# Performance work log

Hardware: AMD Instinct MI355X
Metric: run time of the kernel (lower is better)

## Reference

```python
import jax, jax.numpy as jnp
import numpy as np

B, T, IN = 128, 2048, 32      # batch, seq_len, input dim
S, M = 32, 8                  # kaarma state dim, number of ensemble models
E, H = 64, 128                # encoder dim, controller GRU hidden
CIN = E + 1                   # controller input = [encoded, error]


def setup_inputs() -> dict:
    key = jax.random.key(0)
    ks = jax.random.split(key, 15)
    sc = 0.1  # small init scale keeps tanh/sigmoid in sane range
    return {
        "x": jax.random.normal(ks[0], (B, T, IN), jnp.float32),
        "y": jax.random.normal(ks[1], (B, T), jnp.float32),
        # mkaarma params: shared encoder + per-model recurrent state update
        "W_enc": jax.random.normal(ks[2], (IN, E), jnp.float32) * sc,
        "b_enc": jnp.zeros((E,), jnp.float32),
        "W_in": jax.random.normal(ks[3], (M, IN, S), jnp.float32) * sc,
        "W_rec": jax.random.normal(ks[4], (M, S, S), jnp.float32) * sc,
        "b_s": jnp.zeros((M, S), jnp.float32),
        # controller params: GRU cell + gate head
        "W_x": jax.random.normal(ks[5], (CIN, 3 * H), jnp.float32) * sc,
        "W_h": jax.random.normal(ks[6], (H, 3 * H), jnp.float32) * sc,
        "b_x": jnp.zeros((3 * H,), jnp.float32),
        "b_h": jnp.zeros((3 * H,), jnp.float32),
        "W_gate": jax.random.normal(ks[7], (H, M), jnp.float32) * sc,
        "b_gate": jnp.zeros((M,), jnp.float32),
    }


def reference(x, y, W_enc, b_enc, W_in, W_rec, b_s,
              W_x, W_h, b_x, b_h, W_gate, b_gate):
    Bv = x.shape[0]
    dt = x.dtype

    def step(carry, xy):
        kstate, h, err = carry            # [B,S], [B,H], [B]
        x_t, y_t = xy                     # [B,IN], [B]
        # mkaarma: encode input + ensemble of candidate next states
        encoded = jnp.tanh(x_t @ W_enc + b_enc)                        # [B,E]
        new_state = jnp.tanh(
            jnp.einsum('bi,mis->bms', x_t, W_in)
            + jnp.einsum('bs,msd->bmd', kstate, W_rec)
            + b_s
        )                                                              # [B,M,S]
        # controller: GRU cell on [encoded, error]
        inp = jnp.concatenate([encoded, err[:, None]], axis=1)         # [B,E+1]
        xz, xr, xn = jnp.split(inp @ W_x + b_x, 3, axis=1)
        hz, hr, hn = jnp.split(h @ W_h + b_h, 3, axis=1)
        z = jax.nn.sigmoid(xz + hz)
        r = jax.nn.sigmoid(xr + hr)
        n = jnp.tanh(xn + r * hn)
        h_new = (1.0 - z) * n + z * h                                  # [B,H]
        # gate softmax over models, mix candidate states
        gate = jax.nn.softmax(h_new @ W_gate + b_gate, axis=1)         # [B,M]
        kstate_new = jnp.einsum('bm,bms->bs', gate, new_state)         # [B,S]
        pred = kstate_new[:, -1]                                       # [B]
        err_new = pred - y_t
        return (kstate_new, h_new, err_new), pred

    init = (jnp.zeros((Bv, S), dt), jnp.zeros((Bv, H), dt), jnp.zeros((Bv,), dt))
    xs = (jnp.swapaxes(x, 0, 1), jnp.swapaxes(y, 0, 1))   # time-major
    _, preds = jax.lax.scan(step, init, xs)               # [T,B]
    return jnp.swapaxes(preds, 0, 1)                      # [B,T]
```

## Files before the change

kernel.cpp:

```cpp
#include <hip/hip_runtime.h>

typedef _Float16 h2 __attribute__((ext_vector_type(2)));
typedef _Float16 h8 __attribute__((ext_vector_type(8)));

#define NB 128
#define NT 2048
#define NIN 32
#define NS 32
#define NM 8
#define NE 64
#define NH 128
#define NH3 384

__device__ __forceinline__ h2 mkh2(float a, float b) {
  h2 r; r[0] = (_Float16)a; r[1] = (_Float16)b; return r;
}

template <int I>
__device__ __forceinline__ h2 pick2(h8 v) {
  return __builtin_shufflevector(v, v, 2 * I, 2 * I + 1);
}

__device__ __forceinline__ float fdot2(h2 a, h2 b, float c) {
#if __has_builtin(__builtin_amdgcn_fdot2)
  return __builtin_amdgcn_fdot2(a, b, c, false);
#else
  return c + (float)a[0] * (float)b[0] + (float)a[1] * (float)b[1];
#endif
}

__device__ __forceinline__ float rcpf(float v) {
#if __has_builtin(__builtin_amdgcn_rcpf)
  return __builtin_amdgcn_rcpf(v);
#else
  return 1.0f / v;
#endif
}

__device__ __forceinline__ float sigmoid_f(float v) { return rcpf(1.0f + __expf(-v)); }
__device__ __forceinline__ float tanh_f(float v) { return 1.0f - 2.0f * rcpf(1.0f + __expf(2.0f * v)); }

template <int CTRL>
__device__ __forceinline__ float dppadd(float v) {
  int t = __builtin_amdgcn_update_dpp(0, __float_as_int(v), CTRL, 0xF, 0xF, true);
  return v + __int_as_float(t);
}
__device__ __forceinline__ float wave_reduce63(float v) {
  v = dppadd<0x111>(v); v = dppadd<0x112>(v); v = dppadd<0x114>(v);
  v = dppadd<0x118>(v); v = dppadd<0x142>(v); v = dppadd<0x143>(v);
  return v;
}
__device__ __forceinline__ float pairsum(float v) {
  int t = __builtin_amdgcn_update_dpp(0, __float_as_int(v), 0xB1, 0xF, 0xF, true);
  return v + __int_as_float(t);
}

__device__ __forceinline__ void lds_fence() {
  asm volatile("s_waitcnt lgkmcnt(0)" ::: "memory");
}

__device__ __forceinline__ void softbar() {
  asm volatile("s_waitcnt lgkmcnt(0)\n\ts_barrier" ::: "memory");
}

#define RPW 16
__global__ __launch_bounds__(256, 1) void pre2(
    const float* __restrict__ gx, const float* __restrict__ W_enc,
    const float* __restrict__ b_enc, const float* __restrict__ W_x,
    const float* __restrict__ b_x, _Float16* __restrict__ xpre,
    _Float16* __restrict__ xh16, int t0, int CH) {
  const int tid = threadIdx.x, wv = tid >> 6, lane = tid & 63;
  __shared__ __align__(16) _Float16 x16[4][NIN];
  __shared__ __align__(16) _Float16 encA[4][RPW][NE];

  h2 we[16];
#pragma unroll
  for (int i = 0; i < 16; ++i)
    we[i] = mkh2(W_enc[(2 * i) * NE + lane], W_enc[(2 * i + 1) * NE + lane]);
  const float be = b_enc[lane];

  const int g0 = ((int)blockIdx.x * 4 + wv) * RPW;

  h2 wx3[96];
#pragma unroll 1
  for (int pass = 0; pass < 2; ++pass) {
#pragma unroll
    for (int kk = 0; kk < 3; ++kk) {
      const int j = lane + 64 * (3 * pass + kk);
#pragma unroll
      for (int i = 0; i < 32; ++i)
        wx3[kk * 32 + i] = mkh2(W_x[(size_t)(2 * i) * NH3 + j], W_x[(size_t)(2 * i + 1) * NH3 + j]);
    }
#pragma unroll 1
    for (int r = 0; r < RPW; ++r) {
      const int g = g0 + r;
      const int bb = g / CH, tc = g % CH;
      if (pass == 0) {
        const float* xr = gx + ((size_t)bb * NT + t0 + tc) * NIN;
        if (lane < NIN) x16[wv][lane] = (_Float16)xr[lane];
        lds_fence();
        if (lane < 16) {
          const unsigned v = *(const unsigned*)&x16[wv][2 * lane];
          ((unsigned*)xh16)[(size_t)g * 16 + lane] = v;
        }
        const h8* xv8 = (const h8*)x16[wv];
        float a = be;
#pragma unroll
        for (int i = 0; i < 4; ++i) {
          const h8 xv = xv8[i];
          a = fdot2(pick2<0>(xv), we[4 * i + 0], a);
          a = fdot2(pick2<1>(xv), we[4 * i + 1], a);
          a = fdot2(pick2<2>(xv), we[4 * i + 2], a);
          a = fdot2(pick2<3>(xv), we[4 * i + 3], a);
        }
        encA[wv][r][lane] = (_Float16)tanh_f(a);
        lds_fence();
      }
      const h8* ev8 = (const h8*)encA[wv][r];
      h8 ev[8];
#pragma unroll
      for (int i = 0; i < 8; ++i) ev[i] = ev8[i];
#pragma unroll
      for (int kk = 0; kk < 3; ++kk) {
        const int j = lane + 64 * (3 * pass + kk);
        float a = b_x[j], c = 0.f;
#pragma unroll
        for (int i = 0; i < 8; ++i) {
          a = fdot2(pick2<0>(ev[i]), wx3[kk * 32 + 4 * i + 0], a);
          c = fdot2(pick2<1>(ev[i]), wx3[kk * 32 + 4 * i + 1], c);
          a = fdot2(pick2<2>(ev[i]), wx3[kk * 32 + 4 * i + 2], a);
          c = fdot2(pick2<3>(ev[i]), wx3[kk * 32 + 4 * i + 3], c);
        }
        xpre[(size_t)g * NH3 + j] = (_Float16)(a + c);
      }
    }
  }
}

__global__ __launch_bounds__(384, 2) void rnn8(
    const float* __restrict__ gy, const _Float16* __restrict__ xpre,
    const _Float16* __restrict__ xh16,
    const float* __restrict__ W_h, const float* __restrict__ b_h,
    const float* __restrict__ W_in, const float* __restrict__ W_rec,
    const float* __restrict__ b_s, const float* __restrict__ W_x,
    const float* __restrict__ W_gate, const float* __restrict__ b_gate,
    float* __restrict__ out, float* __restrict__ state, int t0, int CH) {
  const int tid = threadIdx.x;
  const int b = blockIdx.x;
  const int wv = tid >> 6;
  const int lane = tid & 63;

  __shared__ __align__(16) _Float16 h_sh[2][NH];
  __shared__ __align__(16) _Float16 xpre_sh[2][NH3];
  __shared__ __align__(16) float ns_sh[2][NS][NM];
  __shared__ __align__(16) float xd_sh[2][2 * NH];
  __shared__ __align__(16) float gp_sh[2][4][NM];
  __shared__ __align__(16) _Float16 kst_sh[NS];
  __shared__ float err_sh;
  __shared__ float y_lds[NT];

  float* st = state + b * (NH + NS + 1);

  h2 wbig[96];
  h2 wrec[16];
  float wg[8];
  float bh[3], wxe[3];
  float bs4[4];
  float bg[8];
  float h_prev = 0.f;
  unsigned xpq[12];
  h8 xr0[4], xr1[4], xr2[4], xr3[4];

  const int gl = tid - 128;
  const int j = gl >> 1;
  const int half = gl & 1;

  for (int i = tid; i < CH; i += 384) y_lds[i] = gy[(size_t)b * NT + t0 + i];

  if (wv >= 2) {
#pragma unroll
    for (int g = 0; g < 3; ++g) {
      const int jc = j + 128 * g;
#pragma unroll
      for (int i = 0; i < 32; ++i)
        wbig[g * 32 + i] = mkh2(W_h[(size_t)(64 * half + 2 * i) * NH3 + jc],
                                W_h[(size_t)(64 * half + 2 * i + 1) * NH3 + jc]);
      bh[g] = b_h[jc];
      wxe[g] = W_x[(size_t)NE * NH3 + jc];
    }
#pragma unroll
    for (int m = 0; m < 8; ++m) wg[m] = half ? 0.f : W_gate[j * NM + m];
    {
      const int m0 = gl >> 5, d0 = gl & 31;
#pragma unroll
      for (int i = 0; i < 16; ++i)
        wrec[i] = mkh2(W_rec[m0 * 1024 + (2 * i) * 32 + d0],
                       W_rec[m0 * 1024 + (2 * i + 1) * 32 + d0]);
    }
    h_prev = t0 ? st[j] : 0.f;
    if (!half) h_sh[1][j] = (_Float16)h_prev;
  } else if (wv == 1) {
#pragma unroll
    for (int k = 0; k < 4; ++k) {
      const int o = lane + 64 * k, m = o >> 5, d = o & 31;
#pragma unroll
      for (int i = 0; i < 16; ++i)
        wbig[k * 16 + i] = mkh2(W_in[m * 1024 + (2 * i) * 32 + d],
                                W_in[m * 1024 + (2 * i + 1) * 32 + d]);
      bs4[k] = b_s[o];
    }
    {
      const h8* x0 = (const h8*)(xh16 + (size_t)(b * CH) * NIN);
#pragma unroll
      for (int i = 0; i < 4; ++i) xr0[i] = x0[i];
#pragma unroll
      for (int k = 0; k < 4; ++k) {
        float s = bs4[k];
#pragma unroll
        for (int i = 0; i < 4; ++i) {
          s = fdot2(pick2<0>(xr0[i]), wbig[k * 16 + 4 * i + 0], s);
          s = fdot2(pick2<1>(xr0[i]), wbig[k * 16 + 4 * i + 1], s);
          s = fdot2(pick2<2>(xr0[i]), wbig[k * 16 + 4 * i + 2], s);
          s = fdot2(pick2<3>(xr0[i]), wbig[k * 16 + 4 * i + 3], s);
        }
        xd_sh[1][lane + 64 * k] = s;
      }
    }
  } else {
#pragma unroll
    for (int m = 0; m < 8; ++m) bg[m] = b_gate[m];
    if (lane < NS) kst_sh[lane] = t0 ? (_Float16)st[NH + lane] : (_Float16)0.f;
    if (lane == 0) err_sh = t0 ? st[NH + NS] : 0.f;
  }
  __syncthreads();

  float hz = 0.f, hr = 0.f, hn = 0.f;

#define STEPK(K, XRK)                                                          \
  {                                                                            \
    const int tc = tc4 + (K);                                                  \
    const int q = (K) & 1, qp = q ^ 1;                                         \
                                 \
    if (wv >= 2) {                                                             \
      const h8* hv8 = (const h8*)&h_sh[qp][64 * half];                         \
      float a0 = 0.f, c0 = 0.f, a1 = 0.f, c1 = 0.f, a2 = 0.f, c2 = 0.f;        \
      _Pragma("unroll")                                                        \
      for (int i = 0; i < 8; ++i) {                                            \
        const h8 hv = hv8[i];                                                  \
        a0 = fdot2(pick2<0>(hv), wbig[4 * i + 0], a0);                         \
        c0 = fdot2(pick2<1>(hv), wbig[4 * i + 1], c0);                         \
        a0 = fdot2(pick2<2>(hv), wbig[4 * i + 2], a0);                         \
        c0 = fdot2(pick2<3>(hv), wbig[4 * i + 3], c0);                         \
        a1 = fdot2(pick2<0>(hv), wbig[32 + 4 * i + 0], a1);                    \
        c1 = fdot2(pick2<1>(hv), wbig[32 + 4 * i + 1], c1);                    \
        a1 = fdot2(pick2<2>(hv), wbig[32 + 4 * i + 2], a1);                    \
        c1 = fdot2(pick2<3>(hv), wbig[32 + 4 * i + 3], c1);                    \
        a2 = fdot2(pick2<0>(hv), wbig[64 + 4 * i + 0], a2);                    \
        c2 = fdot2(pick2<1>(hv), wbig[64 + 4 * i + 1], c2);                    \
        a2 = fdot2(pick2<2>(hv), wbig[64 + 4 * i + 2], a2);                    \
        c2 = fdot2(pick2<3>(hv), wbig[64 + 4 * i + 3], c2);                    \
      }                                                                        \
      hz = pairsum(a0 + c0) + bh[0];                                           \
      hr = pairsum(a1 + c1) + bh[1];                                           \
      hn = pairsum(a2 + c2) + bh[2];                                           \
    } else if (wv == 0) {                                                      \
      if (tc > 0) {                                                            \
        const int u = lane & 31;                                               \
        const float4* nsv = (const float4*)&ns_sh[qp][u][0];                   \
        const float4 n0 = nsv[0], n1 = nsv[1];                                 \
        const float4* g4 = (const float4*)&gp_sh[qp][0][0];                    \
        float4 A = g4[0], Bv = g4[1];                                          \
        A.x += g4[2].x + g4[4].x + g4[6].x; A.y += g4[2].y + g4[4].y + g4[6].y;\
        A.z += g4[2].z + g4[4].z + g4[6].z; A.w += g4[2].w + g4[4].w + g4[6].w;\
        Bv.x += g4[3].x + g4[5].x + g4[7].x; Bv.y += g4[3].y + g4[5].y + g4[7].y;\
        Bv.z += g4[3].z + g4[5].z + g4[7].z; Bv.w += g4[3].w + g4[5].w + g4[7].w;\
        float l[8] = {A.x + bg[0], A.y + bg[1], A.z + bg[2], A.w + bg[3],      \
                      Bv.x + bg[4], Bv.y + bg[5], Bv.z + bg[6], Bv.w + bg[7]}; \
        float mx = fmaxf(fmaxf(fmaxf(l[0], l[1]), fmaxf(l[2], l[3])),          \
                         fmaxf(fmaxf(l[4], l[5]), fmaxf(l[6], l[7])));         \
        float e[8], s = 0.f;                                                   \
        _Pragma("unroll")                                                      \
        for (int m = 0; m < 8; ++m) { e[m] = __expf(l[m] - mx); s += e[m]; }   \
        float ks = e[0] * n0.x + e[1] * n0.y + e[2] * n0.z + e[3] * n0.w +     \
                   e[4] * n1.x + e[5] * n1.y + e[6] * n1.z + e[7] * n1.w;      \
        ks *= rcpf(s);                                                         \
        if (lane < NS) kst_sh[u] = (_Float16)ks;                               \
        if (lane == 31) {                                                      \
          out[(size_t)b * NT + t0 + tc - 1] = ks;                              \
          err_sh = ks - y_lds[tc - 1];                                         \
        }                                                                      \
      }                                                                        \
    } else {    \
      if ((K) == 0) {                                                          \
        const unsigned* xpg = (const unsigned*)xpre;                           \
        _Pragma("unroll")                                                      \
        for (int k = 0; k < 4; ++k) {                                          \
          const size_t rr = (size_t)(b * CH + tc4 + k) * 192;                  \
          xpq[3 * k + 0] = xpg[rr + lane];                                     \
          xpq[3 * k + 1] = xpg[rr + lane + 64];                                \
          xpq[3 * k + 2] = xpg[rr + lane + 128];                               \
        }                                                                      \
        const h8* xg0 = (const h8*)(xh16 + (size_t)(b * CH + min(tc4 + 1, CH - 1)) * NIN); \
        const h8* xg1 = (const h8*)(xh16 + (size_t)(b * CH + min(tc4 + 2, CH - 1)) * NIN); \
        const h8* xg2 = (const h8*)(xh16 + (size_t)(b * CH + min(tc4 + 3, CH - 1)) * NIN); \
        const h8* xg3 = (const h8*)(xh16 + (size_t)(b * CH + min(tc4 + 4, CH - 1)) * NIN); \
        _Pragma("unroll")                                                      \
        for (int i = 0; i < 4; ++i) {                                          \
          xr0[i] = xg0[i]; xr1[i] = xg1[i]; xr2[i] = xg2[i]; xr3[i] = xg3[i];  \
        }                                                                      \
      }                                                                        \
      unsigned* xps = (unsigned*)&xpre_sh[q][0];                               \
      xps[lane] = xpq[3 * (K) + 0];                                            \
      xps[lane + 64] = xpq[3 * (K) + 1];                                       \
      xps[lane + 128] = xpq[3 * (K) + 2];                                      \
    }                                                                          \
    softbar();                                                                 \
                                 \
    if (wv >= 2) {                                                             \
      const float err = err_sh;                                                \
      const float xz = (float)xpre_sh[q][j] + err * wxe[0];                    \
      const float xr = (float)xpre_sh[q][j + 128] + err * wxe[1];              \
      const float xn = (float)xpre_sh[q][j + 256] + err * wxe[2];              \
      const float z = sigmoid_f(hz + xz);                                      \
      const float r = sigmoid_f(hr + xr);                                      \
      const float n = tanh_f(xn + r * hn);                                     \
      const float hnew = (1.f - z) * n + z * h_prev;                           \
      h_prev = hnew;                                                           \
      if (!half) h_sh[q][j] = (_Float16)hnew;                                  \
      float p[8];                                                              \
      _Pragma("unroll")                                                        \
      for (int m = 0; m < 8; ++m) p[m] = wave_reduce63(hnew * wg[m]);          \
      if (lane == 63) {                                                        \
        *(float4*)&gp_sh[q][wv - 2][0] = make_float4(p[0], p[1], p[2], p[3]);  \
        *(float4*)&gp_sh[q][wv - 2][4] = make_float4(p[4], p[5], p[6], p[7]);  \
      }                                                                        \
      const h8* kv8 = (const h8*)kst_sh;                                       \
      float s = xd_sh[qp][gl];                                                 \
      _Pragma("unroll")                                                        \
      for (int i = 0; i < 4; ++i) {                                            \
        const h8 kv = kv8[i];                                                  \
        s = fdot2(pick2<0>(kv), wrec[4 * i + 0], s);                           \
        s = fdot2(pick2<1>(kv), wrec[4 * i + 1], s);                           \
        s = fdot2(pick2<2>(kv), wrec[4 * i + 2], s);                           \
        s = fdot2(pick2<3>(kv), wrec[4 * i + 3], s);                           \
      }                                                                        \
      ns_sh[q][gl & 31][gl >> 5] = tanh_f(s);                                  \
    } else if (wv == 1) {                                                      \
      if (tc + 1 < CH) {                                                       \
        _Pragma("unroll")                                                      \
        for (int k = 0; k < 4; ++k) {                                          \
          float s = bs4[k];                                                    \
          _Pragma("unroll")                                                    \
          for (int i = 0; i < 4; ++i) {                                        \
            s = fdot2(pick2<0>(XRK[i]), wbig[k * 16 + 4 * i + 0], s);          \
            s = fdot2(pick2<1>(XRK[i]), wbig[k * 16 + 4 * i + 1], s);          \
            s = fdot2(pick2<2>(XRK[i]), wbig[k * 16 + 4 * i + 2], s);          \
            s = fdot2(pick2<3>(XRK[i]), wbig[k * 16 + 4 * i + 3], s);          \
          }                                                                    \
          xd_sh[q][lane + 64 * k] = s;                                         \
        }                                                                      \
      }                                                                        \
    }                                                                          \
    softbar();                                                                 \
  }

  for (int tc4 = 0; tc4 < CH; tc4 += 4) {
    STEPK(0, xr0)
    STEPK(1, xr1)
    STEPK(2, xr2)
    STEPK(3, xr3)
  }
#undef STEPK

  if (wv == 0) {
    const int qf = (CH - 1) & 1;
    const int u = lane & 31;
    const float4* nsv = (const float4*)&ns_sh[qf][u][0];
    const float4 n0 = nsv[0], n1 = nsv[1];
    const float4* g4 = (const float4*)&gp_sh[qf][0][0];
    float4 A = g4[0], Bv = g4[1];
    A.x += g4[2].x + g4[4].x + g4[6].x; A.y += g4[2].y + g4[4].y + g4[6].y;
    A.z += g4[2].z + g4[4].z + g4[6].z; A.w += g4[2].w + g4[4].w + g4[6].w;
    Bv.x += g4[3].x + g4[5].x + g4[7].x; Bv.y += g4[3].y + g4[5].y + g4[7].y;
    Bv.z += g4[3].z + g4[5].z + g4[7].z; Bv.w += g4[3].w + g4[5].w + g4[7].w;
    float l[8] = {A.x + bg[0], A.y + bg[1], A.z + bg[2], A.w + bg[3],
                  Bv.x + bg[4], Bv.y + bg[5], Bv.z + bg[6], Bv.w + bg[7]};
    float mx = fmaxf(fmaxf(fmaxf(l[0], l[1]), fmaxf(l[2], l[3])),
                     fmaxf(fmaxf(l[4], l[5]), fmaxf(l[6], l[7])));
    float e[8], s = 0.f;
#pragma unroll
    for (int m = 0; m < 8; ++m) { e[m] = __expf(l[m] - mx); s += e[m]; }
    float ks = e[0] * n0.x + e[1] * n0.y + e[2] * n0.z + e[3] * n0.w +
               e[4] * n1.x + e[5] * n1.y + e[6] * n1.z + e[7] * n1.w;
    ks *= rcpf(s);
    if (lane < NS) st[NH + u] = ks;
    if (lane == 31) {
      out[(size_t)b * NT + t0 + CH - 1] = ks;
      st[NH + NS] = ks - y_lds[CH - 1];
    }
  }
  if (wv >= 2 && !half) st[j] = h_prev;
}

extern "C" void kernel_launch(void* const* d_in, const int* in_sizes, int n_in,
                              void* d_out, int out_size, void* d_ws, size_t ws_size,
                              hipStream_t stream) {
  const float* x = (const float*)d_in[0];
  const float* y = (const float*)d_in[1];
  const float* W_enc = (const float*)d_in[2];
  const float* b_enc = (const float*)d_in[3];
  const float* W_in = (const float*)d_in[4];
  const float* W_rec = (const float*)d_in[5];
  const float* b_s = (const float*)d_in[6];
  const float* W_x = (const float*)d_in[7];
  const float* W_h = (const float*)d_in[8];
  const float* b_x = (const float*)d_in[9];
  const float* b_h = (const float*)d_in[10];
  const float* W_gate = (const float*)d_in[11];
  const float* b_gate = (const float*)d_in[12];
  float* out = (float*)d_out;

  const size_t stateB = (size_t)NB * (NH + NS + 1) * sizeof(float);
  int CH = NT;
  while (CH > 4) {
    const size_t need = (size_t)NB * CH * NH3 * 2 + (size_t)NB * CH * NIN * 2 + stateB;
    if (need <= ws_size) break;
    CH >>= 1;
  }

  _Float16* xpre = (_Float16*)d_ws;
  _Float16* xh16 = (_Float16*)((char*)d_ws + (size_t)NB * CH * NH3 * 2);
  float* state = (float*)((char*)d_ws + (size_t)NB * CH * NH3 * 2 + (size_t)NB * CH * NIN * 2);

  for (int t0 = 0; t0 < NT; t0 += CH) {
    pre2<<<dim3(2 * CH), dim3(256), 0, stream>>>(
        x, W_enc, b_enc, W_x, b_x, xpre, xh16, t0, CH);
    rnn8<<<dim3(NB), dim3(384), 0, stream>>>(
        y, xpre, xh16, W_h, b_h, W_in, W_rec, b_s, W_x, W_gate, b_gate,
        out, state, t0, CH);
  }
}
```

Before: 2.610 ms.

## Prefetch xpre directly into GRU registers and restructure precompute kernel loops

The recurrent kernel no longer stages xpre through LDS via wave 1. Each GRU lane now loads its own three fp16 xpre values from global memory four steps ahead, and the xh16 prefetch moves to the end of the step. Wave priority is raised during the W_h matvec, and the ns_sh layout is transposed to [M][S]. The precompute kernel doubles rows per wave, software-prefetches the next x row and encoder row, and splits the accumulator chains. The aim is to take LDS staging and one wave's serial work off the per-step critical path, at the cost of more global-load latency exposure and extra registers.

```diff
diff --git a/kernel.cpp b/kernel.cpp
--- a/kernel.cpp
+++ b/kernel.cpp
@@ -40,6 +40,12 @@
 __device__ __forceinline__ float sigmoid_f(float v) { return rcpf(1.0f + __expf(-v)); }
 __device__ __forceinline__ float tanh_f(float v) { return 1.0f - 2.0f * rcpf(1.0f + __expf(2.0f * v)); }
 
+__device__ __forceinline__ float f16bits_tof(unsigned short u) {
+  _Float16 h;
+  __builtin_memcpy(&h, &u, 2);
+  return (float)h;
+}
+
 template <int CTRL>
 __device__ __forceinline__ float dppadd(float v) {
   int t = __builtin_amdgcn_update_dpp(0, __float_as_int(v), CTRL, 0xF, 0xF, true);
@@ -58,12 +64,11 @@
 __device__ __forceinline__ void lds_fence() {
   asm volatile("s_waitcnt lgkmcnt(0)" ::: "memory");
 }
-
 __device__ __forceinline__ void softbar() {
   asm volatile("s_waitcnt lgkmcnt(0)\n\ts_barrier" ::: "memory");
 }
 
-#define RPW 16
+#define RPW 32
 __global__ __launch_bounds__(256, 1) void pre2(
     const float* __restrict__ gx, const float* __restrict__ W_enc,
     const float* __restrict__ b_enc, const float* __restrict__ W_x,
@@ -82,6 +87,7 @@
   const int g0 = ((int)blockIdx.x * 4 + wv) * RPW;
 
   h2 wx3[96];
+  float bx3[3];
 #pragma unroll 1
   for (int pass = 0; pass < 2; ++pass) {
 #pragma unroll
@@ -90,54 +96,89 @@
 #pragma unroll
       for (int i = 0; i < 32; ++i)
         wx3[kk * 32 + i] = mkh2(W_x[(size_t)(2 * i) * NH3 + j], W_x[(size_t)(2 * i + 1) * NH3 + j]);
-    }
+      bx3[kk] = b_x[j];
+    }
+    if (pass == 0) {
+      int bb = g0 / CH, tcc = g0 % CH;
+      float xreg = 0.f;
+      if (lane < NIN) xreg = gx[((size_t)bb * NT + t0 + tcc) * NIN + lane];
 #pragma unroll 1
-    for (int r = 0; r < RPW; ++r) {
-      const int g = g0 + r;
-      const int bb = g / CH, tc = g % CH;
-      if (pass == 0) {
-        const float* xr = gx + ((size_t)bb * NT + t0 + tc) * NIN;
-        if (lane < NIN) x16[wv][lane] = (_Float16)xr[lane];
+      for (int r = 0; r < RPW; ++r) {
+        const int g = g0 + r;
+        if (lane < NIN) x16[wv][lane] = (_Float16)xreg;
+        int bb2 = bb, tc2 = tcc + 1;
+        if (tc2 == CH) { tc2 = 0; ++bb2; }
+        if (r + 1 < RPW && lane < NIN)
+          xreg = gx[((size_t)bb2 * NT + t0 + tc2) * NIN + lane];
         lds_fence();
         if (lane < 16) {
           const unsigned v = *(const unsigned*)&x16[wv][2 * lane];
           ((unsigned*)xh16)[(size_t)g * 16 + lane] = v;
         }
         const h8* xv8 = (const h8*)x16[wv];
-        float a = be;
+        float a = be, c = 0.f;
 #pragma unroll
         for (int i = 0; i < 4; ++i) {
           const h8 xv = xv8[i];
           a = fdot2(pick2<0>(xv), we[4 * i + 0], a);
-          a = fdot2(pick2<1>(xv), we[4 * i + 1], a);
+          c = fdot2(pick2<1>(xv), we[4 * i + 1], c);
           a = fdot2(pick2<2>(xv), we[4 * i + 2], a);
-          a = fdot2(pick2<3>(xv), we[4 * i + 3], a);
+          c = fdot2(pick2<3>(xv), we[4 * i + 3], c);
         }
-        encA[wv][r][lane] = (_Float16)tanh_f(a);
+        encA[wv][r][lane] = (_Float16)tanh_f(a + c);
         lds_fence();
+        const h8* ev8 = (const h8*)encA[wv][r];
+        h8 ev[8];
+#pragma unroll
+        for (int i = 0; i < 8; ++i) ev[i] = ev8[i];
+#pragma unroll
+        for (int kk = 0; kk < 3; ++kk) {
+          float a0 = bx3[kk], c0 = 0.f;
+#pragma unroll
+          for (int i = 0; i < 8; ++i) {
+            a0 = fdot2(pick2<0>(ev[i]), wx3[kk * 32 + 4 * i + 0], a0);
+            c0 = fdot2(pick2<1>(ev[i]), wx3[kk * 32 + 4 * i + 1], c0);
+            a0 = fdot2(pick2<2>(ev[i]), wx3[kk * 32 + 4 * i + 2], a0);
+            c0 = fdot2(pick2<3>(ev[i]), wx3[kk * 32 + 4 * i + 3], c0);
+          }
+          xpre[(size_t)g * NH3 + lane + 64 * kk] = (_Float16)(a0 + c0);
+        }
+        bb = bb2; tcc = tc2;
       }
-      const h8* ev8 = (const h8*)encA[wv][r];
-      h8 ev[8];
-#pragma unroll
-      for (int i = 0; i < 8; ++i) ev[i] = ev8[i];
-#pragma unroll
-      for (int kk = 0; kk < 3; ++kk) {
-        const int j = lane + 64 * (3 * pass + kk);
-        float a = b_x[j], c = 0.f;
-#pragma unroll
-        for (int i = 0; i < 8; ++i) {
-          a = fdot2(pick2<0>(ev[i]), wx3[kk * 32 + 4 * i + 0], a);
-          c = fdot2(pick2<1>(ev[i]), wx3[kk * 32 + 4 * i + 1], c);
-          a = fdot2(pick2<2>(ev[i]), wx3[kk * 32 + 4 * i + 2], a);
-          c = fdot2(pick2<3>(ev[i]), wx3[kk * 32 + 4 * i + 3], c);
+    } else {
+      h8 ev[8], evn[8];
+      {
+        const h8* e8 = (const h8*)encA[wv][0];
+#pragma unroll
+        for (int i = 0; i < 8; ++i) ev[i] = e8[i];
+      }
+#pragma unroll 1
+      for (int r = 0; r < RPW; ++r) {
+        if (r + 1 < RPW) {
+          const h8* e8 = (const h8*)encA[wv][r + 1];
+#pragma unroll
+          for (int i = 0; i < 8; ++i) evn[i] = e8[i];
         }
-        xpre[(size_t)g * NH3 + j] = (_Float16)(a + c);
+#pragma unroll
+        for (int kk = 0; kk < 3; ++kk) {
+          float a0 = bx3[kk], c0 = 0.f;
+#pragma unroll
+          for (int i = 0; i < 8; ++i) {
+            a0 = fdot2(pick2<0>(ev[i]), wx3[kk * 32 + 4 * i + 0], a0);
+            c0 = fdot2(pick2<1>(ev[i]), wx3[kk * 32 + 4 * i + 1], c0);
+            a0 = fdot2(pick2<2>(ev[i]), wx3[kk * 32 + 4 * i + 2], a0);
+            c0 = fdot2(pick2<3>(ev[i]), wx3[kk * 32 + 4 * i + 3], c0);
+          }
+          xpre[(size_t)(g0 + r) * NH3 + lane + 64 * (3 + kk)] = (_Float16)(a0 + c0);
+        }
+#pragma unroll
+        for (int i = 0; i < 8; ++i) ev[i] = evn[i];
       }
     }
   }
 }
 
-__global__ __launch_bounds__(384, 2) void rnn8(
+__global__ __launch_bounds__(384, 2) void rnn10(
     const float* __restrict__ gy, const _Float16* __restrict__ xpre,
     const _Float16* __restrict__ xh16,
     const float* __restrict__ W_h, const float* __restrict__ b_h,
@@ -151,8 +192,7 @@
   const int lane = tid & 63;
 
   __shared__ __align__(16) _Float16 h_sh[2][NH];
-  __shared__ __align__(16) _Float16 xpre_sh[2][NH3];
-  __shared__ __align__(16) float ns_sh[2][NS][NM];
+  __shared__ __align__(16) float ns_sh[2][NM][NS];
   __shared__ __align__(16) float xd_sh[2][2 * NH];
   __shared__ __align__(16) float gp_sh[2][4][NM];
   __shared__ __align__(16) _Float16 kst_sh[NS];
@@ -168,7 +208,7 @@
   float bs4[4];
   float bg[8];
   float h_prev = 0.f;
-  unsigned xpq[12];
+  unsigned short xp[4][3];
   h8 xr0[4], xr1[4], xr2[4], xr3[4];
 
   const int gl = tid - 128;
@@ -196,6 +236,16 @@
       for (int i = 0; i < 16; ++i)
         wrec[i] = mkh2(W_rec[m0 * 1024 + (2 * i) * 32 + d0],
                        W_rec[m0 * 1024 + (2 * i + 1) * 32 + d0]);
+    }
+    {
+      const unsigned short* xpg = (const unsigned short*)xpre;
+#pragma unroll
+      for (int k = 0; k < 4; ++k) {
+        const size_t base = (size_t)(b * CH + min(k, CH - 1)) * NH3;
+        xp[k][0] = xpg[base + j];
+        xp[k][1] = xpg[base + j + 128];
+        xp[k][2] = xpg[base + j + 256];
+      }
     }
     h_prev = t0 ? st[j] : 0.f;
     if (!half) h_sh[1][j] = (_Float16)h_prev;
@@ -242,6 +292,7 @@
     const int q = (K) & 1, qp = q ^ 1;                                         \
                                  \
     if (wv >= 2) {                                                             \
+      __builtin_amdgcn_s_setprio(1);                                           \
       const h8* hv8 = (const h8*)&h_sh[qp][64 * half];                         \
       float a0 = 0.f, c0 = 0.f, a1 = 0.f, c1 = 0.f, a2 = 0.f, c2 = 0.f;        \
       _Pragma("unroll")                                                        \
@@ -263,11 +314,13 @@
       hz = pairsum(a0 + c0) + bh[0];                                           \
       hr = pairsum(a1 + c1) + bh[1];                                           \
       hn = pairsum(a2 + c2) + bh[2];                                           \
+      __builtin_amdgcn_s_setprio(0);                                           \
     } else if (wv == 0) {                                                      \
       if (tc > 0) {                                                            \
         const int u = lane & 31;                                               \
-        const float4* nsv = (const float4*)&ns_sh[qp][u][0];                   \
-        const float4 n0 = nsv[0], n1 = nsv[1];                                 \
+        float nsv[8];                                                          \
+        _Pragma("unroll")                                                      \
+        for (int m = 0; m < 8; ++m) nsv[m] = ns_sh[qp][m][u];                  \
         const float4* g4 = (const float4*)&gp_sh[qp][0][0];                    \
         float4 A = g4[0], Bv = g4[1];                                          \
         A.x += g4[2].x + g4[4].x + g4[6].x; A.y += g4[2].y + g4[4].y + g4[6].y;\
@@ -281,8 +334,9 @@
         float e[8], s = 0.f;                                                   \
         _Pragma("unroll")                                                      \
         for (int m = 0; m < 8; ++m) { e[m] = __expf(l[m] - mx); s += e[m]; }   \
-        float ks = e[0] * n0.x + e[1] * n0.y + e[2] * n0.z + e[3] * n0.w +     \
-                   e[4] * n1.x + e[5] * n1.y + e[6] * n1.z + e[7] * n1.w;      \
+        float ks = 0.f;                                                        \
+        _Pragma("unroll")                                                      \
+        for (int m = 0; m < 8; ++m) ks += e[m] * nsv[m];                       \
         ks *= rcpf(s);                                                         \
         if (lane < NS) kst_sh[u] = (_Float16)ks;                               \
         if (lane == 31) {                                                      \
@@ -290,37 +344,14 @@
           err_sh = ks - y_lds[tc - 1];                                         \
         }                                                                      \
       }                                                                        \
-    } else {    \
-      if ((K) == 0) {                                                          \
-        const unsigned* xpg = (const unsigned*)xpre;                           \
-        _Pragma("unroll")                                                      \
-        for (int k = 0; k < 4; ++k) {                                          \
-          const size_t rr = (size_t)(b * CH + tc4 + k) * 192;                  \
-          xpq[3 * k + 0] = xpg[rr + lane];                                     \
-          xpq[3 * k + 1] = xpg[rr + lane + 64];                                \
-          xpq[3 * k + 2] = xpg[rr + lane + 128];                               \
-        }                                                                      \
-        const h8* xg0 = (const h8*)(xh16 + (size_t)(b * CH + min(tc4 + 1, CH - 1)) * NIN); \
-        const h8* xg1 = (const h8*)(xh16 + (size_t)(b * CH + min(tc4 + 2, CH - 1)) * NIN); \
-        const h8* xg2 = (const h8*)(xh16 + (size_t)(b * CH + min(tc4 + 3, CH - 1)) * NIN); \
-        const h8* xg3 = (const h8*)(xh16 + (size_t)(b * CH + min(tc4 + 4, CH - 1)) * NIN); \
-        _Pragma("unroll")                                                      \
-        for (int i = 0; i < 4; ++i) {                                          \
-          xr0[i] = xg0[i]; xr1[i] = xg1[i]; xr2[i] = xg2[i]; xr3[i] = xg3[i];  \
-        }                                                                      \
-      }                                                                        \
-      unsigned* xps = (unsigned*)&xpre_sh[q][0];                               \
-      xps[lane] = xpq[3 * (K) + 0];                                            \
-      xps[lane + 64] = xpq[3 * (K) + 1];                                       \
-      xps[lane + 128] = xpq[3 * (K) + 2];                                      \
-    }                                                                          \
+    }                                                   \
     softbar();                                                                 \
                                  \
     if (wv >= 2) {                                                             \
       const float err = err_sh;                                                \
-      const float xz = (float)xpre_sh[q][j] + err * wxe[0];                    \
-      const float xr = (float)xpre_sh[q][j + 128] + err * wxe[1];              \
-      const float xn = (float)xpre_sh[q][j + 256] + err * wxe[2];              \
+      const float xz = f16bits_tof(xp[K][0]) + err * wxe[0];                   \
+      const float xr = f16bits_tof(xp[K][1]) + err * wxe[1];                   \
+      const float xn = f16bits_tof(xp[K][2]) + err * wxe[2];                   \
       const float z = sigmoid_f(hz + xz);                                      \
       const float r = sigmoid_f(hr + xr);                                      \
       const float n = tanh_f(xn + r * hn);                                     \
@@ -344,7 +375,15 @@
         s = fdot2(pick2<2>(kv), wrec[4 * i + 2], s);                           \
         s = fdot2(pick2<3>(kv), wrec[4 * i + 3], s);                           \
       }                                                                        \
-      ns_sh[q][gl & 31][gl >> 5] = tanh_f(s);                                  \
+      ns_sh[q][gl >> 5][gl & 31] = tanh_f(s);                                  \
+                                                \
+      {                                                                        \
+        const unsigned short* xpg = (const unsigned short*)xpre;               \
+        const size_t base = (size_t)(b * CH + min(tc + 4, CH - 1)) * NH3;      \
+        xp[K][0] = xpg[base + j];                                              \
+        xp[K][1] = xpg[base + j + 128];                                        \
+        xp[K][2] = xpg[base + j + 256];                                        \
+      }                                                                        \
     } else if (wv == 1) {                                                      \
       if (tc + 1 < CH) {                                                       \
         _Pragma("unroll")                                                      \
@@ -360,8 +399,29 @@
           xd_sh[q][lane + 64 * k] = s;                                         \
         }                                                                      \
       }                                                                        \
+      if ((K) == 3) {                      \
+        const h8* xg0 = (const h8*)(xh16 + (size_t)(b * CH + min(tc4 + 5, CH - 1)) * NIN); \
+        const h8* xg1 = (const h8*)(xh16 + (size_t)(b * CH + min(tc4 + 6, CH - 1)) * NIN); \
+        const h8* xg2 = (const h8*)(xh16 + (size_t)(b * CH + min(tc4 + 7, CH - 1)) * NIN); \
+        const h8* xg3 = (const h8*)(xh16 + (size_t)(b * CH + min(tc4 + 8, CH - 1)) * NIN); \
+        _Pragma("unroll")                                                      \
+        for (int i = 0; i < 4; ++i) {                                          \
+          xr0[i] = xg0[i]; xr1[i] = xg1[i]; xr2[i] = xg2[i]; xr3[i] = xg3[i];  \
+        }                                                                      \
+      }                                                                        \
     }                                                                          \
     softbar();                                                                 \
+  }
+
+  if (wv == 1) {
+    const h8* xg0 = (const h8*)(xh16 + (size_t)(b * CH + min(1, CH - 1)) * NIN);
+    const h8* xg1 = (const h8*)(xh16 + (size_t)(b * CH + min(2, CH - 1)) * NIN);
+    const h8* xg2 = (const h8*)(xh16 + (size_t)(b * CH + min(3, CH - 1)) * NIN);
+    const h8* xg3 = (const h8*)(xh16 + (size_t)(b * CH + min(4, CH - 1)) * NIN);
+#pragma unroll
+    for (int i = 0; i < 4; ++i) {
+      xr0[i] = xg0[i]; xr1[i] = xg1[i]; xr2[i] = xg2[i]; xr3[i] = xg3[i];
+    }
   }
 
   for (int tc4 = 0; tc4 < CH; tc4 += 4) {
@@ -375,8 +435,9 @@
   if (wv == 0) {
     const int qf = (CH - 1) & 1;
     const int u = lane & 31;
-    const float4* nsv = (const float4*)&ns_sh[qf][u][0];
-    const float4 n0 = nsv[0], n1 = nsv[1];
+    float nsv[8];
+#pragma unroll
+    for (int m = 0; m < 8; ++m) nsv[m] = ns_sh[qf][m][u];
     const float4* g4 = (const float4*)&gp_sh[qf][0][0];
     float4 A = g4[0], Bv = g4[1];
     A.x += g4[2].x + g4[4].x + g4[6].x; A.y += g4[2].y + g4[4].y + g4[6].y;
@@ -390,8 +451,9 @@
     float e[8], s = 0.f;
 #pragma unroll
     for (int m = 0; m < 8; ++m) { e[m] = __expf(l[m] - mx); s += e[m]; }
-    float ks = e[0] * n0.x + e[1] * n0.y + e[2] * n0.z + e[3] * n0.w +
-               e[4] * n1.x + e[5] * n1.y + e[6] * n1.z + e[7] * n1.w;
+    float ks = 0.f;
+#pragma unroll
+    for (int m = 0; m < 8; ++m) ks += e[m] * nsv[m];
     ks *= rcpf(s);
     if (lane < NS) st[NH + u] = ks;
     if (lane == 31) {
@@ -422,7 +484,7 @@
 
   const size_t stateB = (size_t)NB * (NH + NS + 1) * sizeof(float);
   int CH = NT;
-  while (CH > 4) {
+  while (CH > 8) {
     const size_t need = (size_t)NB * CH * NH3 * 2 + (size_t)NB * CH * NIN * 2 + stateB;
     if (need <= ws_size) break;
     CH >>= 1;
@@ -433,9 +495,9 @@
   float* state = (float*)((char*)d_ws + (size_t)NB * CH * NH3 * 2 + (size_t)NB * CH * NIN * 2);
 
   for (int t0 = 0; t0 < NT; t0 += CH) {
-    pre2<<<dim3(2 * CH), dim3(256), 0, stream>>>(
+    pre2<<<dim3(NB * CH / (4 * RPW)), dim3(256), 0, stream>>>(
         x, W_enc, b_enc, W_x, b_x, xpre, xh16, t0, CH);
-    rnn8<<<dim3(NB), dim3(384), 0, stream>>>(
+    rnn10<<<dim3(NB), dim3(384), 0, stream>>>(
         y, xpre, xh16, W_h, b_h, W_in, W_rec, b_s, W_x, W_gate, b_gate,
         out, state, t0, CH);
   }
```

After: 2.896 ms. 11.0% more time.
